# Kernel optimization log

Hardware: AMD Instinct MI355X
Metric: run time of the kernel (lower is better)

Reference implementation:

```python
import jax, jax.numpy as jnp
import numpy as np

N_NODES = 100000
HIDDEN = 128
E = 524288  # edges per graph (pos and neg)


def setup_inputs() -> dict:
    key = jax.random.key(0)
    ks = jax.random.split(key, 8)
    return {
        "z_src": jax.random.normal(ks[0], (N_NODES, HIDDEN), dtype=jnp.float32),
        "z_dst": jax.random.normal(ks[1], (N_NODES, HIDDEN), dtype=jnp.float32),
        "pos_src": jax.random.randint(ks[2], (E,), 0, N_NODES, dtype=jnp.int64),
        "pos_dst": jax.random.randint(ks[3], (E,), 0, N_NODES, dtype=jnp.int64),
        "neg_src": jax.random.randint(ks[4], (E,), 0, N_NODES, dtype=jnp.int64),
        "neg_dst": jax.random.randint(ks[5], (E,), 0, N_NODES, dtype=jnp.int64),
        "W1": jax.random.normal(ks[6], (2 * HIDDEN, HIDDEN), dtype=jnp.float32) * (1.0 / np.sqrt(2 * HIDDEN)),
        "b1": jnp.zeros((HIDDEN,), dtype=jnp.float32),
        "W2": jax.random.normal(ks[7], (HIDDEN, 1), dtype=jnp.float32) * (1.0 / np.sqrt(HIDDEN)),
        "b2": jnp.zeros((1,), dtype=jnp.float32),
    }


def reference(z_src, z_dst, pos_src, pos_dst, neg_src, neg_dst, W1, b1, W2, b2):
    # Gather endpoint features for pos then neg edges (cat along edge dim)
    src_idx = jnp.concatenate([pos_src, neg_src])  # [2E]
    dst_idx = jnp.concatenate([pos_dst, neg_dst])  # [2E]
    z = jnp.concatenate([z_src[src_idx], z_dst[dst_idx]], axis=-1)  # [2E, 2h]
    z = jax.nn.relu(z @ W1 + b1)  # [2E, h]
    z = z @ W2 + b2               # [2E, 1]
    return z.reshape(-1)
```

## Files before the change

### kernel.cpp

```cpp
#include <hip/hip_runtime.h>
#include <hip/hip_bf16.h>
#include <cstdint>

#define N_NODES 100000
#define HIDDEN  128
#define NEDGE   524288
#define NT      6250
#define PBLK    256
#define WSTRIDE (PBLK * 4)

typedef __attribute__((ext_vector_type(8))) short short8;
typedef __attribute__((ext_vector_type(4))) float f32x4;

__device__ __forceinline__ unsigned short f2b(float f) {
    unsigned u = __float_as_uint(f);
    u += 0x7FFFu + ((u >> 16) & 1u);
    return (unsigned short)(u >> 16);
}
__device__ __forceinline__ float b2f(unsigned x16) {
    return __uint_as_float(x16 << 16);
}

__device__ __forceinline__ void async_copy16(const float* g, float* l) {
    __builtin_amdgcn_global_load_lds(
        (const __attribute__((address_space(1))) unsigned int*)g,
        (__attribute__((address_space(3))) unsigned int*)l,
        16, 0, 0);
}

__global__ void wp_kernel(const float* __restrict__ W1,
                          unsigned short* __restrict__ Wp)
{
    const int f = blockIdx.x;
    const int tb = blockIdx.y;
    const int lane = threadIdx.x;
    const int t = lane & 15, q = lane >> 4;
    const int n = f >> 2, ks = f & 3;
    short8 v;
#pragma unroll
    for (int j = 0; j < 8; ++j)
        v[j] = (short)f2b(W1[(size_t)(tb * 128 + ks * 32 + q * 8 + j) * 128 + n * 16 + t]);
    *(short8*)(Wp + ((size_t)(tb * 32 + f) * 64 + lane) * 8) = v;
}

__global__ __launch_bounds__(256, 2)
void precompute_kernel(const float* __restrict__ z_src,
                       const float* __restrict__ z_dst,
                       const unsigned short* __restrict__ Wp,
                       const float* __restrict__ b1,
                       unsigned short* __restrict__ Asrc,
                       unsigned short* __restrict__ Adst)
{
    const int table = blockIdx.y;
    const float* __restrict__ z = table ? z_dst : z_src;
    unsigned short* __restrict__ A = table ? Adst : Asrc;

    __shared__ float zbuf[4][2][2048];

    const int tid = threadIdx.x;
    const int wave = tid >> 6;
    const int lane = tid & 63;
    const int t = lane & 15;
    const int q = lane >> 4;

    short8 wfrag[32];
    {
        const unsigned short* wp = Wp + ((size_t)table * 32 * 64 + lane) * 8;
#pragma unroll
        for (int f = 0; f < 32; ++f)
            wfrag[f] = *(const short8*)(wp + (size_t)f * 64 * 8);
    }

    float4 b1v[8];
#pragma unroll
    for (int n = 0; n < 8; ++n)
        b1v[n] = (table == 0) ? *(const float4*)(b1 + n * 16 + q * 4)
                              : make_float4(0.f, 0.f, 0.f, 0.f);

    const int lhi = lane >> 5;
    const int llo = lane & 31;
#define STAGE(m0, p)                                                          \
    do {                                                                      \
        _Pragma("unroll")                                                     \
        for (int j = 0; j < 8; ++j) {                                         \
            const int r = j * 2 + lhi;                                        \
            const int c = llo ^ (r & 7);                                      \
            async_copy16(z + (size_t)((m0) + r) * 128 + c * 4,                \
                         &zbuf[wave][p][j * 256]);                            \
        }                                                                     \
    } while (0)

    int tile = blockIdx.x * 4 + wave;
    int p = 0;
    STAGE(tile * 16, 0);
    __builtin_amdgcn_s_waitcnt(0xF70);
    asm volatile("" ::: "memory");

    while (tile < NT) {
        const int m0 = tile * 16;
        const int ntile = tile + WSTRIDE;
        const int nm0 = (ntile < NT ? ntile : tile) * 16;
        STAGE(nm0, p ^ 1);
        asm volatile("" ::: "memory");
        __builtin_amdgcn_s_waitcnt(0xF78);
        asm volatile("" ::: "memory");

        short8 b[4];
#pragma unroll
        for (int ks = 0; ks < 4; ++ks) {
            const int c0 = ks * 8 + 2 * q;
            const int s = t & 7;
            const float4 v0 = *(const float4*)&zbuf[wave][p][(t * 32 + (c0 ^ s)) * 4];
            const float4 v1 = *(const float4*)&zbuf[wave][p][(t * 32 + ((c0 + 1) ^ s)) * 4];
            b[ks][0] = (short)f2b(v0.x); b[ks][1] = (short)f2b(v0.y);
            b[ks][2] = (short)f2b(v0.z); b[ks][3] = (short)f2b(v0.w);
            b[ks][4] = (short)f2b(v1.x); b[ks][5] = (short)f2b(v1.y);
            b[ks][6] = (short)f2b(v1.z); b[ks][7] = (short)f2b(v1.w);
        }

        f32x4 acc[8];
#pragma unroll
        for (int n = 0; n < 8; ++n) acc[n] = (f32x4){0.f, 0.f, 0.f, 0.f};
#pragma unroll
        for (int n = 0; n < 8; ++n)
#pragma unroll
            for (int ks = 0; ks < 4; ++ks)
                acc[n] = __builtin_amdgcn_mfma_f32_16x16x32_bf16(
                             wfrag[n * 4 + ks], b[ks], acc[n], 0, 0, 0);

        unsigned short* ob = (unsigned short*)&zbuf[wave][p][0];
        const int sw = (t & 7) * 2;
#pragma unroll
        for (int n = 0; n < 8; ++n) {
            ushort4 h;
            h.x = f2b(acc[n][0] + b1v[n].x);
            h.y = f2b(acc[n][1] + b1v[n].y);
            h.z = f2b(acc[n][2] + b1v[n].z);
            h.w = f2b(acc[n][3] + b1v[n].w);
            *(ushort4*)&ob[t * 136 + (((n * 4 + q) ^ sw) * 4)] = h;
        }
        const int rr = lane >> 4;
#pragma unroll
        for (int it = 0; it < 4; ++it) {
            const int r = it * 4 + rr;
            const uint4 v = *(const uint4*)&ob[r * 136 + (((2 * t) ^ ((r & 7) * 2)) * 4)];
            *(uint4*)(A + (size_t)(m0 + r) * 128 + t * 8) = v;
        }
        asm volatile("" ::: "memory");

        p ^= 1;
        tile = ntile;
    }
#undef STAGE
}

__global__ __launch_bounds__(256, 7)
void edge_kernel(const unsigned short* __restrict__ Asrc,
                 const unsigned short* __restrict__ Adst,
                 const int* __restrict__ pos_src,
                 const int* __restrict__ pos_dst,
                 const int* __restrict__ neg_src,
                 const int* __restrict__ neg_dst,
                 const float* __restrict__ W2,
                 const float* __restrict__ b2,
                 float* __restrict__ out)
{
    const int tid = threadIdx.x;
    const int t = tid & 15;
    const int g = tid >> 4;

    const bool is_pos = blockIdx.x < 8192;
    const int* __restrict__ sp = is_pos ? pos_src : neg_src;
    const int* __restrict__ dp = is_pos ? pos_dst : neg_dst;
    const int eb = (is_pos ? (int)blockIdx.x : (int)blockIdx.x - 8192) * 64;

    float w2r[8];
#pragma unroll
    for (int j = 0; j < 8; ++j) w2r[j] = W2[t * 8 + j];
    const float bias2 = b2[0];

    unsigned soff[4], doff[4];
#pragma unroll
    for (int i = 0; i < 4; ++i) {
        soff[i] = ((unsigned)sp[eb + i * 16 + g] << 8) + t * 16;
        doff[i] = ((unsigned)dp[eb + i * 16 + g] << 8) + t * 16;
    }

    const unsigned char* As = (const unsigned char*)Asrc;
    const unsigned char* Ad = (const unsigned char*)Adst;

    uint4 ua[4], ub[4];
#pragma unroll
    for (int i = 0; i < 4; ++i) {
        ua[i] = *(const uint4*)(As + soff[i]);
        ub[i] = *(const uint4*)(Ad + doff[i]);
    }
    asm volatile("" ::: "memory");

#define CHUNK(i, vm)                                                          \
    do {                                                                      \
        __builtin_amdgcn_s_waitcnt(0xF70 | (vm));                             \
        asm volatile("" ::: "memory");                                        \
        const unsigned* pa = (const unsigned*)&ua[i];                         \
        const unsigned* pb = (const unsigned*)&ub[i];                         \
        float acc = 0.f;                                                      \
        _Pragma("unroll")                                                     \
        for (int j2 = 0; j2 < 4; ++j2) {                                      \
            float h0 = b2f(pa[j2] & 0xFFFFu) + b2f(pb[j2] & 0xFFFFu);         \
            float h1 = b2f(pa[j2] >> 16)     + b2f(pb[j2] >> 16);             \
            h0 = fmaxf(h0, 0.f);                                              \
            h1 = fmaxf(h1, 0.f);                                              \
            acc = fmaf(h0, w2r[2 * j2], acc);                                 \
            acc = fmaf(h1, w2r[2 * j2 + 1], acc);                             \
        }                                                                     \
        acc += __shfl_xor(acc, 1);                                            \
        acc += __shfl_xor(acc, 2);                                            \
        acc += __shfl_xor(acc, 4);                                            \
        acc += __shfl_xor(acc, 8);                                            \
        if (t == 0) out[blockIdx.x * 64 + (i) * 16 + g] = acc + bias2;        \
    } while (0)

    CHUNK(0, 6);
    CHUNK(1, 4);
    CHUNK(2, 2);
    CHUNK(3, 0);
#undef CHUNK
}

extern "C" void kernel_launch(void* const* d_in, const int* in_sizes, int n_in,
                              void* d_out, int out_size, void* d_ws, size_t ws_size,
                              hipStream_t stream) {
    const float* z_src  = (const float*)d_in[0];
    const float* z_dst  = (const float*)d_in[1];
    const int* pos_src  = (const int*)d_in[2];
    const int* pos_dst  = (const int*)d_in[3];
    const int* neg_src  = (const int*)d_in[4];
    const int* neg_dst  = (const int*)d_in[5];
    const float* W1     = (const float*)d_in[6];
    const float* b1     = (const float*)d_in[7];
    const float* W2     = (const float*)d_in[8];
    const float* b2     = (const float*)d_in[9];
    float* out = (float*)d_out;

    unsigned short* Asrc = (unsigned short*)d_ws;
    unsigned short* Adst = Asrc + (size_t)N_NODES * HIDDEN;
    unsigned short* Wp   = Adst + (size_t)N_NODES * HIDDEN;

    wp_kernel<<<dim3(32, 2), 64, 0, stream>>>(W1, Wp);

    precompute_kernel<<<dim3(PBLK, 2), 256, 0, stream>>>(z_src, z_dst, Wp, b1,
                                                         Asrc, Adst);

    edge_kernel<<<16384, 256, 0, stream>>>(Asrc, Adst, pos_src, pos_dst,
                                           neg_src, neg_dst, W2, b2, out);
}
```

Before: 220.9 us.

## Fuse weight prep, node precompute, and edge scoring into one cooperative kernel

Replaces the three-kernel sequence with a single cooperative kernel of 512 blocks. Each block converts its W1 half to bf16 fragments from LDS, runs the per-node projection, then waits on a grid-wide sync and scores 2048 edges with a persistent loop. This removes two kernel launches and the Wp round trip, at the cost of a grid barrier and only 512 resident blocks for the gather-bound edge phase. The original three-kernel path is kept as a fallback if the cooperative launch fails.

```diff
diff --git a/kernel.cpp b/kernel.cpp
--- a/kernel.cpp
+++ b/kernel.cpp
@@ -1,6 +1,9 @@
 #include <hip/hip_runtime.h>
 #include <hip/hip_bf16.h>
+#include <hip/hip_cooperative_groups.h>
 #include <cstdint>
+
+namespace cg = cooperative_groups;
 
 #define N_NODES 100000
 #define HIDDEN  128
@@ -28,33 +31,21 @@
         16, 0, 0);
 }
 
-__global__ void wp_kernel(const float* __restrict__ W1,
-                          unsigned short* __restrict__ Wp)
+__global__ __launch_bounds__(256, 2)
+void fused_kernel(const float* __restrict__ z_src,
+                  const float* __restrict__ z_dst,
+                  const int* __restrict__ pos_src,
+                  const int* __restrict__ pos_dst,
+                  const int* __restrict__ neg_src,
+                  const int* __restrict__ neg_dst,
+                  const float* __restrict__ W1,
+                  const float* __restrict__ b1,
+                  const float* __restrict__ W2,
+                  const float* __restrict__ b2,
+                  unsigned short* __restrict__ Asrc,
+                  unsigned short* __restrict__ Adst,
+                  float* __restrict__ out)
 {
-    const int f = blockIdx.x;
-    const int tb = blockIdx.y;
-    const int lane = threadIdx.x;
-    const int t = lane & 15, q = lane >> 4;
-    const int n = f >> 2, ks = f & 3;
-    short8 v;
-#pragma unroll
-    for (int j = 0; j < 8; ++j)
-        v[j] = (short)f2b(W1[(size_t)(tb * 128 + ks * 32 + q * 8 + j) * 128 + n * 16 + t]);
-    *(short8*)(Wp + ((size_t)(tb * 32 + f) * 64 + lane) * 8) = v;
-}
-
-__global__ __launch_bounds__(256, 2)
-void precompute_kernel(const float* __restrict__ z_src,
-                       const float* __restrict__ z_dst,
-                       const unsigned short* __restrict__ Wp,
-                       const float* __restrict__ b1,
-                       unsigned short* __restrict__ Asrc,
-                       unsigned short* __restrict__ Adst)
-{
-    const int table = blockIdx.y;
-    const float* __restrict__ z = table ? z_dst : z_src;
-    unsigned short* __restrict__ A = table ? Adst : Asrc;
-
     __shared__ float zbuf[4][2][2048];
 
     const int tid = threadIdx.x;
@@ -62,14 +53,34 @@
     const int lane = tid & 63;
     const int t = lane & 15;
     const int q = lane >> 4;
-
+    const int b = (int)blockIdx.x;
+    const int table = b & 1;
+    const int bx = b >> 1;
+
+    const float* __restrict__ z = table ? z_dst : z_src;
+    unsigned short* __restrict__ A = table ? Adst : Asrc;
+
+    float* lin = &zbuf[0][0][0];
+    {
+        const float* Wh = W1 + (size_t)table * 128 * 128;
+#pragma unroll
+        for (int r = 0; r < 16; ++r)
+            async_copy16(Wh + r * 1024 + wave * 256 + lane * 4,
+                         lin + r * 1024 + wave * 256);
+        __builtin_amdgcn_s_waitcnt(0xF70);
+        __syncthreads();
+    }
     short8 wfrag[32];
-    {
-        const unsigned short* wp = Wp + ((size_t)table * 32 * 64 + lane) * 8;
-#pragma unroll
-        for (int f = 0; f < 32; ++f)
-            wfrag[f] = *(const short8*)(wp + (size_t)f * 64 * 8);
-    }
+#pragma unroll
+    for (int f = 0; f < 32; ++f) {
+        const int n = f >> 2, ks = f & 3;
+        short8 v;
+#pragma unroll
+        for (int j = 0; j < 8; ++j)
+            v[j] = (short)f2b(lin[(ks * 32 + q * 8 + j) * 128 + n * 16 + t]);
+        wfrag[f] = v;
+    }
+    __syncthreads();
 
     float4 b1v[8];
 #pragma unroll
@@ -90,6 +101,196 @@
         }                                                                     \
     } while (0)
 
+    int tile = bx * 4 + wave;
+    int p = 0;
+    STAGE(tile * 16, 0);
+    __builtin_amdgcn_s_waitcnt(0xF70);
+    asm volatile("" ::: "memory");
+
+    while (tile < NT) {
+        const int m0 = tile * 16;
+        const int ntile = tile + WSTRIDE;
+        const int nm0 = (ntile < NT ? ntile : tile) * 16;
+        STAGE(nm0, p ^ 1);
+        asm volatile("" ::: "memory");
+        __builtin_amdgcn_s_waitcnt(0xF78);
+        asm volatile("" ::: "memory");
+
+        short8 bb[4];
+#pragma unroll
+        for (int ks = 0; ks < 4; ++ks) {
+            const int c0 = ks * 8 + 2 * q;
+            const int s = t & 7;
+            const float4 v0 = *(const float4*)&zbuf[wave][p][(t * 32 + (c0 ^ s)) * 4];
+            const float4 v1 = *(const float4*)&zbuf[wave][p][(t * 32 + ((c0 + 1) ^ s)) * 4];
+            bb[ks][0] = (short)f2b(v0.x); bb[ks][1] = (short)f2b(v0.y);
+            bb[ks][2] = (short)f2b(v0.z); bb[ks][3] = (short)f2b(v0.w);
+            bb[ks][4] = (short)f2b(v1.x); bb[ks][5] = (short)f2b(v1.y);
+            bb[ks][6] = (short)f2b(v1.z); bb[ks][7] = (short)f2b(v1.w);
+        }
+
+        f32x4 acc[8];
+#pragma unroll
+        for (int n = 0; n < 8; ++n) acc[n] = (f32x4){0.f, 0.f, 0.f, 0.f};
+#pragma unroll
+        for (int n = 0; n < 8; ++n)
+#pragma unroll
+            for (int ks = 0; ks < 4; ++ks)
+                acc[n] = __builtin_amdgcn_mfma_f32_16x16x32_bf16(
+                             wfrag[n * 4 + ks], bb[ks], acc[n], 0, 0, 0);
+
+        unsigned short* ob = (unsigned short*)&zbuf[wave][p][0];
+        const int sw = (t & 7) * 2;
+#pragma unroll
+        for (int n = 0; n < 8; ++n) {
+            ushort4 h;
+            h.x = f2b(acc[n][0] + b1v[n].x);
+            h.y = f2b(acc[n][1] + b1v[n].y);
+            h.z = f2b(acc[n][2] + b1v[n].z);
+            h.w = f2b(acc[n][3] + b1v[n].w);
+            *(ushort4*)&ob[t * 136 + (((n * 4 + q) ^ sw) * 4)] = h;
+        }
+        const int rr = lane >> 4;
+#pragma unroll
+        for (int it = 0; it < 4; ++it) {
+            const int r = it * 4 + rr;
+            const uint4 v = *(const uint4*)&ob[r * 136 + (((2 * t) ^ ((r & 7) * 2)) * 4)];
+            *(uint4*)(A + (size_t)(m0 + r) * 128 + t * 8) = v;
+        }
+        asm volatile("" ::: "memory");
+
+        p ^= 1;
+        tile = ntile;
+    }
+#undef STAGE
+
+    __threadfence();
+    cg::this_grid().sync();
+
+    const bool is_pos = b < 256;
+    const int* __restrict__ sp = is_pos ? pos_src : neg_src;
+    const int* __restrict__ dp = is_pos ? pos_dst : neg_dst;
+    const int ebase = (b & 255) * 2048;
+    const int eg = tid >> 4;
+
+    float w2r[8];
+#pragma unroll
+    for (int j = 0; j < 8; ++j) w2r[j] = W2[t * 8 + j];
+    const float bias2 = b2[0];
+
+    const unsigned char* As = (const unsigned char*)Asrc;
+    const unsigned char* Ad = (const unsigned char*)Adst;
+
+    for (int rnd = 0; rnd < 32; ++rnd) {
+        const int e0 = ebase + rnd * 64;
+        unsigned soff[4], doff[4];
+#pragma unroll
+        for (int i = 0; i < 4; ++i) {
+            soff[i] = ((unsigned)sp[e0 + i * 16 + eg] << 8) + t * 16;
+            doff[i] = ((unsigned)dp[e0 + i * 16 + eg] << 8) + t * 16;
+        }
+        uint4 ua[4], ub[4];
+#pragma unroll
+        for (int i = 0; i < 4; ++i) {
+            ua[i] = *(const uint4*)(As + soff[i]);
+            ub[i] = *(const uint4*)(Ad + doff[i]);
+        }
+        asm volatile("" ::: "memory");
+
+#define CHUNK(i, vm)                                                          \
+    do {                                                                      \
+        __builtin_amdgcn_s_waitcnt(0xF70 | (vm));                             \
+        asm volatile("" ::: "memory");                                        \
+        const unsigned* pa = (const unsigned*)&ua[i];                         \
+        const unsigned* pb = (const unsigned*)&ub[i];                         \
+        float acc = 0.f;                                                      \
+        _Pragma("unroll")                                                     \
+        for (int j2 = 0; j2 < 4; ++j2) {                                      \
+            float h0 = b2f(pa[j2] & 0xFFFFu) + b2f(pb[j2] & 0xFFFFu);         \
+            float h1 = b2f(pa[j2] >> 16)     + b2f(pb[j2] >> 16);             \
+            h0 = fmaxf(h0, 0.f);                                              \
+            h1 = fmaxf(h1, 0.f);                                              \
+            acc = fmaf(h0, w2r[2 * j2], acc);                                 \
+            acc = fmaf(h1, w2r[2 * j2 + 1], acc);                             \
+        }                                                                     \
+        acc += __shfl_xor(acc, 1);                                            \
+        acc += __shfl_xor(acc, 2);                                            \
+        acc += __shfl_xor(acc, 4);                                            \
+        acc += __shfl_xor(acc, 8);                                            \
+        if (t == 0)                                                           \
+            out[(size_t)b * 2048 + rnd * 64 + (i) * 16 + eg] = acc + bias2;   \
+    } while (0)
+
+        CHUNK(0, 6);
+        CHUNK(1, 4);
+        CHUNK(2, 2);
+        CHUNK(3, 0);
+#undef CHUNK
+    }
+}
+
+__global__ void wp_kernel(const float* __restrict__ W1,
+                          unsigned short* __restrict__ Wp)
+{
+    const int f = blockIdx.x;
+    const int tb = blockIdx.y;
+    const int lane = threadIdx.x;
+    const int t = lane & 15, q = lane >> 4;
+    const int n = f >> 2, ks = f & 3;
+    short8 v;
+#pragma unroll
+    for (int j = 0; j < 8; ++j)
+        v[j] = (short)f2b(W1[(size_t)(tb * 128 + ks * 32 + q * 8 + j) * 128 + n * 16 + t]);
+    *(short8*)(Wp + ((size_t)(tb * 32 + f) * 64 + lane) * 8) = v;
+}
+
+__global__ __launch_bounds__(256, 2)
+void precompute_kernel(const float* __restrict__ z_src,
+                       const float* __restrict__ z_dst,
+                       const unsigned short* __restrict__ Wp,
+                       const float* __restrict__ b1,
+                       unsigned short* __restrict__ Asrc,
+                       unsigned short* __restrict__ Adst)
+{
+    const int table = blockIdx.y;
+    const float* __restrict__ z = table ? z_dst : z_src;
+    unsigned short* __restrict__ A = table ? Adst : Asrc;
+
+    __shared__ float zbuf[4][2][2048];
+
+    const int tid = threadIdx.x;
+    const int wave = tid >> 6;
+    const int lane = tid & 63;
+    const int t = lane & 15;
+    const int q = lane >> 4;
+
+    short8 wfrag[32];
+    {
+        const unsigned short* wp = Wp + ((size_t)table * 32 * 64 + lane) * 8;
+#pragma unroll
+        for (int f = 0; f < 32; ++f)
+            wfrag[f] = *(const short8*)(wp + (size_t)f * 64 * 8);
+    }
+
+    float4 b1v[8];
+#pragma unroll
+    for (int n = 0; n < 8; ++n)
+        b1v[n] = (table == 0) ? *(const float4*)(b1 + n * 16 + q * 4)
+                              : make_float4(0.f, 0.f, 0.f, 0.f);
+
+    const int lhi = lane >> 5;
+    const int llo = lane & 31;
+#define STAGE(m0, p)                                                          \
+    do {                                                                      \
+        _Pragma("unroll")                                                     \
+        for (int j = 0; j < 8; ++j) {                                         \
+            const int r = j * 2 + lhi;                                        \
+            const int c = llo ^ (r & 7);                                      \
+            async_copy16(z + (size_t)((m0) + r) * 128 + c * 4,                \
+                         &zbuf[wave][p][j * 256]);                            \
+        }                                                                     \
+    } while (0)
+
     int tile = blockIdx.x * 4 + wave;
     int p = 0;
     STAGE(tile * 16, 0);
@@ -105,17 +306,17 @@
         __builtin_amdgcn_s_waitcnt(0xF78);
         asm volatile("" ::: "memory");
 
-        short8 b[4];
+        short8 bb[4];
 #pragma unroll
         for (int ks = 0; ks < 4; ++ks) {
             const int c0 = ks * 8 + 2 * q;
             const int s = t & 7;
             const float4 v0 = *(const float4*)&zbuf[wave][p][(t * 32 + (c0 ^ s)) * 4];
             const float4 v1 = *(const float4*)&zbuf[wave][p][(t * 32 + ((c0 + 1) ^ s)) * 4];
-            b[ks][0] = (short)f2b(v0.x); b[ks][1] = (short)f2b(v0.y);
-            b[ks][2] = (short)f2b(v0.z); b[ks][3] = (short)f2b(v0.w);
-            b[ks][4] = (short)f2b(v1.x); b[ks][5] = (short)f2b(v1.y);
-            b[ks][6] = (short)f2b(v1.z); b[ks][7] = (short)f2b(v1.w);
+            bb[ks][0] = (short)f2b(v0.x); bb[ks][1] = (short)f2b(v0.y);
+            bb[ks][2] = (short)f2b(v0.z); bb[ks][3] = (short)f2b(v0.w);
+            bb[ks][4] = (short)f2b(v1.x); bb[ks][5] = (short)f2b(v1.y);
+            bb[ks][6] = (short)f2b(v1.z); bb[ks][7] = (short)f2b(v1.w);
         }
 
         f32x4 acc[8];
@@ -126,7 +327,7 @@
 #pragma unroll
             for (int ks = 0; ks < 4; ++ks)
                 acc[n] = __builtin_amdgcn_mfma_f32_16x16x32_bf16(
-                             wfrag[n * 4 + ks], b[ks], acc[n], 0, 0, 0);
+                             wfrag[n * 4 + ks], bb[ks], acc[n], 0, 0, 0);
 
         unsigned short* ob = (unsigned short*)&zbuf[wave][p][0];
         const int sw = (t & 7) * 2;
@@ -246,11 +447,20 @@
     unsigned short* Adst = Asrc + (size_t)N_NODES * HIDDEN;
     unsigned short* Wp   = Adst + (size_t)N_NODES * HIDDEN;
 
-    wp_kernel<<<dim3(32, 2), 64, 0, stream>>>(W1, Wp);
-
-    precompute_kernel<<<dim3(PBLK, 2), 256, 0, stream>>>(z_src, z_dst, Wp, b1,
-                                                         Asrc, Adst);
-
-    edge_kernel<<<16384, 256, 0, stream>>>(Asrc, Adst, pos_src, pos_dst,
-                                           neg_src, neg_dst, W2, b2, out);
-}
+    void* args[13] = {
+        (void*)&z_src, (void*)&z_dst,
+        (void*)&pos_src, (void*)&pos_dst, (void*)&neg_src, (void*)&neg_dst,
+        (void*)&W1, (void*)&b1, (void*)&W2, (void*)&b2,
+        (void*)&Asrc, (void*)&Adst, (void*)&out
+    };
+    hipError_t e = hipLaunchCooperativeKernel((const void*)fused_kernel,
+                                              dim3(512), dim3(256),
+                                              args, 0u, stream);
+    if (e != hipSuccess) {
+        wp_kernel<<<dim3(32, 2), 64, 0, stream>>>(W1, Wp);
+        precompute_kernel<<<dim3(PBLK, 2), 256, 0, stream>>>(z_src, z_dst, Wp,
+                                                             b1, Asrc, Adst);
+        edge_kernel<<<16384, 256, 0, stream>>>(Asrc, Adst, pos_src, pos_dst,
+                                               neg_src, neg_dst, W2, b2, out);
+    }
+}
```

New measurement: 416.4 us. 88.5% more time.
